# Optimization experiments

Hardware: AMD Instinct MI355X
Metric: run time of the kernel (lower is better)

Reference implementation:

```python
import jax, jax.numpy as jnp
import numpy as np

B, S, E, H, VS, VT = 128, 256, 512, 512, 32000, 32000


def _lstm_layer(x, mask, Wih, Whh, bih, bhh):
    # x: (S,B,E_in), mask: (S,B) bool. PyTorch gate order i,f,g,o.
    h0 = jnp.zeros((x.shape[1], Whh.shape[1]), x.dtype)
    c0 = h0
    def step(carry, inp):
        h, c = carry
        xt, mt = inp
        g = xt @ Wih.T + h @ Whh.T + bih + bhh
        i, f, gg, o = jnp.split(g, 4, axis=-1)
        i = jax.nn.sigmoid(i); f = jax.nn.sigmoid(f)
        gg = jnp.tanh(gg); o = jax.nn.sigmoid(o)
        c_new = f * c + i * gg
        h_new = o * jnp.tanh(c_new)
        m = mt[:, None]
        h2 = jnp.where(m, h_new, h)
        c2 = jnp.where(m, c_new, c)
        return (h2, c2), jnp.where(m, h_new, 0.0)  # pad_packed zero-pads
    (hT, cT), ys = jax.lax.scan(step, (h0, c0), (x, mask))
    return ys, cT


def setup_inputs() -> dict:
    key = jax.random.key(0)
    ks = jax.random.split(key, 32)
    def w(k, shape, fan_in):
        bound = 1.0 / np.sqrt(fan_in)
        return jax.random.uniform(k, shape, jnp.float32, -bound, bound)
    src_tokens = jax.random.randint(ks[0], (B, S), 0, VS)
    src_lens = jnp.sort(jax.random.randint(ks[1], (B,), S // 2, S + 1))[::-1]
    src_lens = src_lens.at[0].set(S)  # pack_padded expects descending, max = S
    trg_tokens = jax.random.randint(ks[2], (B,), 0, VT)
    inp = {
        'src_tokens': src_tokens, 'src_lens': src_lens, 'trg_tokens': trg_tokens,
        'src_emb': jax.random.normal(ks[3], (VS, E), jnp.float32),
        'trg_emb': jax.random.normal(ks[4], (VT, E), jnp.float32),
        'enc_Wih0': w(ks[5], (4 * H, E), H), 'enc_Whh0': w(ks[6], (4 * H, H), H),
        'enc_bih0': w(ks[7], (4 * H,), H), 'enc_bhh0': w(ks[8], (4 * H,), H),
        'enc_Wih1': w(ks[9], (4 * H, H), H), 'enc_Whh1': w(ks[10], (4 * H, H), H),
        'enc_bih1': w(ks[11], (4 * H,), H), 'enc_bhh1': w(ks[12], (4 * H,), H),
        'dec_Wih': w(ks[13], (4 * H, E + H), H), 'dec_Whh': w(ks[14], (4 * H, H), H),
        'dec_bih': w(ks[15], (4 * H,), H), 'dec_bhh': w(ks[16], (4 * H,), H),
        'W_init': w(ks[17], (H, 2 * H), 2 * H), 'b_init': w(ks[18], (H,), 2 * H),
        'W_hid': w(ks[19], (H, 2 * H), 2 * H), 'b_hid': w(ks[20], (H,), 2 * H),
        'W_out': w(ks[21], (VT, H), H), 'b_out': w(ks[22], (VT,), H),
    }
    return inp


def reference(src_tokens, src_lens, trg_tokens, src_emb, trg_emb,
              enc_Wih0, enc_Whh0, enc_bih0, enc_bhh0,
              enc_Wih1, enc_Whh1, enc_bih1, enc_bhh1,
              dec_Wih, dec_Whh, dec_bih, dec_bhh,
              W_init, b_init, W_hid, b_hid, W_out, b_out):
    # ---- encode ----
    x = src_emb[src_tokens]                       # (B,S,E)
    x = jnp.transpose(x, (1, 0, 2))               # (S,B,E)
    mask = jnp.arange(S)[:, None] < src_lens[None, :]  # (S,B)
    y0, c0f = _lstm_layer(x, mask, enc_Wih0, enc_Whh0, enc_bih0, enc_bhh0)
    y1, c1f = _lstm_layer(y0, mask, enc_Wih1, enc_Whh1, enc_bih1, enc_bhh1)
    src_states = jnp.transpose(y1, (1, 0, 2))     # (B,S,H)
    # final cell states (num_layers,B,H) -> (B, num_layers*H)
    final_cells = jnp.concatenate([c0f, c1f], axis=-1)  # (B,2H)
    c_dec = final_cells @ W_init.T + b_init       # (B,H)
    h_dec = jnp.tanh(c_dec)
    # ---- one decoder step ----
    emb_t = trg_emb[trg_tokens]                   # (B,E)
    vec = jnp.concatenate([emb_t, jnp.zeros((B, H), emb_t.dtype)], axis=-1)
    g = vec @ dec_Wih.T + h_dec @ dec_Whh.T + dec_bih + dec_bhh
    i, f, gg, o = jnp.split(g, 4, axis=-1)
    c = jax.nn.sigmoid(f) * c_dec + jax.nn.sigmoid(i) * jnp.tanh(gg)
    h = jax.nn.sigmoid(o) * jnp.tanh(c)           # (B,H)
    # ---- masked dot attention ----
    scores = jnp.einsum('bsh,bh->bs', src_states, h)
    smask = jnp.arange(S)[None, :] < src_lens[:, None]
    scores = jnp.where(smask, scores, -jnp.inf)
    attw = jax.nn.softmax(scores, axis=-1)
    context = jnp.einsum('bs,bsh->bh', attw, src_states)
    attn_vec = jnp.concatenate([h, context], axis=-1) @ W_hid.T + b_hid
    logits = attn_vec @ W_out.T + b_out
    prd_token = jnp.argmax(logits, axis=-1)       # softmax is monotone
    return context, h, prd_token
```

## Files before the change

### kernel.cpp

```cpp
#include <hip/hip_runtime.h>
#include <stdint.h>


typedef _Float16 f16;
typedef f16 f16x8 __attribute__((ext_vector_type(8)));
typedef float f32x4 __attribute__((ext_vector_type(4)));

#define LOSCALE 2048.0f
#define LOINV   (1.0f/2048.0f)

#define B_  128
#define S_  256
#define H_  512

__device__ __forceinline__ uint16_t hbits(f16 h){ union{ f16 f; uint16_t u; } c; c.f=h; return c.u; }
__device__ __forceinline__ float f16val(uint16_t u){ union{ uint16_t u; f16 f; } c; c.u=u; return (float)c.f; }

__device__ __forceinline__ uint32_t split_ph2(float x){
  f16 h = (f16)x;
  float r = (x - (float)h) * LOSCALE;
  return (uint32_t)hbits(h) | ((uint32_t)hbits((f16)r) << 16);
}
__device__ __forceinline__ float ph2val(uint32_t p){
  union{ uint16_t u; f16 f; } a, b; a.u = (uint16_t)p; b.u = (uint16_t)(p>>16);
// ... 116 lines not shown

  for (int it = 0; it < 8; ++it) {
    __syncthreads();
    {
      const uint32_t* gsrc = (wv < 2 ? Ab : Wb) + (size_t)it*8192 + (size_t)(wv & 1)*4096;
      uint32_t* lb = (uint32_t*)(sm + (size_t)wv*16384);
#pragma unroll
      for (int e = 0; e < 16; ++e)
        gload_lds16(gsrc + e*256, lb + e*256, lane);
    }
    asm volatile("s_waitcnt vmcnt(0)" ::: "memory");
    __syncthreads();

#pragma unroll
    for (int kt = 0; kt < 2; ++kt) {
      uint4 ah[4], al[4];
#pragma unroll
      for (int i = 0; i < 4; ++i) {
        const uint8_t* p = sm + (size_t)(kt*8 + wm*4 + i)*2048 + lane*16;
        ah[i] = *(const uint4*)p; al[i] = *(const uint4*)(p + 1024);
      }
#pragma unroll
      for (int j = 0; j < 4; ++j) {
        const uint8_t* p = sm + 32768 + (size_t)(kt*8 + wn*4 + j)*2048 + lane*16;
        uint4 bh = *(const uint4*)p;
        uint4 bl = *(const uint4*)(p + 1024);
#pragma unroll
        for (int i = 0; i < 4; ++i) {
          acc0[i][j] = mfma16(ah[i], bh, acc0[i][j]);
          acc1[i][j] = mfma16(al[i], bh, acc1[i][j]);
          acc1[i][j] = mfma16(ah[i], bl, acc1[i][j]);
        }
      }
    }
  }

#pragma unroll
  for (int i = 0; i < 4; ++i) {
    int row0 = bm0 + (wm*4+i)*16 + ((lane>>4)<<2);
#pragma unroll
    for (int j = 0; j < 4; ++j) {
      int col = bn0 + (wn*4+j)*16 + (lane & 15);
      float bias = 0.f;
      if (b0) bias += b0[col];
      if (b1) bias += b1[col];
      f32x4 v = acc0[i][j] + acc1[i][j] * LOINV;
#pragma unroll
      for (int r = 0; r < 4; ++r) {
        size_t idx = (size_t)(row0 + r) * N + col;
        float out = v[r] + bias;
        if (addC) out += C[idx];
        if (outMode == 2) ((uint16_t*)C)[idx] = hbits((f16)out);
        else              C[idx] = out;
      }
    }
  }
}

__global__ __launch_bounds__(256,2) void k_gemm(
    const uint32_t* __restrict__ A, int lda,
    const float* __restrict__ W, int ldw,
    const float* __restrict__ b0, const float* __restrict__ b1,
    float* __restrict__ C, int N, int K, int addC)
{
  __shared__ uint8_t sm[65536];
  const int tid = threadIdx.x;
  const int lane = tid & 63, wv = tid >> 6;
  const int wm = wv >> 1, wn = wv & 1;
  const int bn0 = blockIdx.x * 128, bm0 = blockIdx.y * 128;

  const int srow = tid >> 1;
  const int skh  = (tid & 1) * 32;
  const int smt  = srow >> 4, sr = srow & 15, skt = tid & 1;

  f32x4 acc0[4][4], acc1[4][4];
#pragma unroll
  for (int i = 0; i < 4; ++i)
#pragma unroll
    for (int j = 0; j < 4; ++j) { acc0[i][j] = (f32x4){0,0,0,0}; acc1[i][j] = (f32x4){0,0,0,0}; }

  for (int k0 = 0; k0 < K; k0 += 64) {
    __syncthreads();
    {
      const uint32_t* ap = A + (size_t)(bm0 + srow) * lda + (k0 + skh);
      uint4 q[8];
#pragma unroll
      for (int e = 0; e < 8; ++e) q[e] = *(const uint4*)(ap + e*4);
#pragma unroll
      for (int kg = 0; kg < 4; ++kg) {
        uint4 hi, lo; pack_hi_lo(q[2*kg], q[2*kg+1], hi, lo);
        uint8_t* dst = sm + (size_t)(smt*2 + skt)*2048 + (size_t)(sr + 16*kg)*16;
        *(uint4*)dst = hi; *(uint4*)(dst + 1024) = lo;
      }
    }
    {
      const float* wp = W + (size_t)(bn0 + srow) * ldw + (k0 + skh);
      float xs[32];
#pragma unroll
      for (int e = 0; e < 8; ++e) { float4 v = *(const float4*)(wp + e*4);
        xs[e*4+0]=v.x; xs[e*4+1]=v.y; xs[e*4+2]=v.z; xs[e*4+3]=v.w; }
#pragma unroll
      for (int kg = 0; kg < 4; ++kg) {
        uint4 hi, lo; split_pack8(xs + kg*8, hi, lo);
        uint8_t* dst = sm + 32768 + (size_t)(smt*2 + skt)*2048 + (size_t)(sr + 16*kg)*16;
        *(uint4*)dst = hi; *(uint4*)(dst + 1024) = lo;
      }
    }
    __syncthreads();

#pragma unroll
    for (int kt = 0; kt < 2; ++kt) {
      uint4 ah[4], al[4];
#pragma unroll
      for (int i = 0; i < 4; ++i) {
        const uint8_t* p = sm + (size_t)(((wm*4+i)*2 + kt))*2048 + lane*16;
        ah[i] = *(const uint4*)p; al[i] = *(const uint4*)(p + 1024);
      }
#pragma unroll
      for (int j = 0; j < 4; ++j) {
        const uint8_t* p = sm + 32768 + (size_t)(((wn*4+j)*2 + kt))*2048 + lane*16;
        uint4 bh = *(const uint4*)p;
        uint4 bl = *(const uint4*)(p + 1024);
#pragma unroll
        for (int i = 0; i < 4; ++i) {
          acc0[i][j] = mfma16(ah[i], bh, acc0[i][j]);
          acc1[i][j] = mfma16(al[i], bh, acc1[i][j]);
          acc1[i][j] = mfma16(ah[i], bl, acc1[i][j]);
        }
      }
    }
  }

#pragma unroll
  for (int i = 0; i < 4; ++i) {
    int row0 = bm0 + (wm*4+i)*16 + ((lane>>4)<<2);
#pragma unroll
    for (int j = 0; j < 4; ++j) {
      int col = bn0 + (wn*4+j)*16 + (lane & 15);
      float bias = 0.f;
      if (b0) bias += b0[col];
      if (b1) bias += b1[col];
      f32x4 v = acc0[i][j] + acc1[i][j] * LOINV;
#pragma unroll
      for (int r = 0; r < 4; ++r) {
        size_t idx = (size_t)(row0 + r) * N + col;
        float out = v[r] + bias;
        if (addC) out += C[idx];
        C[idx] = out;
      }
    }
  }
}

__global__ __launch_bounds__(256,1) void k_lstm2(
    const float* __restrict__ Whh0, const float* __restrict__ Whh1,
    const float* __restrict__ bih1, const float* __restrict__ bhh1,
    const uint16_t* __restrict__ xg,
    const int*  __restrict__ lens,
    uint32_t* __restrict__ mb0,
    uint32_t* __restrict__ mb1,
    float* __restrict__ cb0, float* __restrict__ cb1,
    uint32_t* __restrict__ y1buf,
    uint32_t* __restrict__ flg0, uint32_t* __restrict__ flg1,
    uint32_t* __restrict__ xcdclaim,
    const uint32_t* __restrict__ Wp1,
    int s0, int nt)
{
  __shared__ uint8_t sm[139264];
  uint8_t* wih   = sm;
  uint8_t* tileA = sm + 65536;
  uint8_t* tileB = sm + 98304;
  uint64_t* tA64 = (uint64_t*)tileA;
  uint64_t* tB64 = (uint64_t*)tileB;
  float* g0ex = (float*)(sm + 131072);
  float* g1ex = (float*)(sm + 135168);

  const int tid = threadIdx.x, lane = tid & 63, wv = tid >> 6;
  const int row = lane & 15, qh = lane >> 4;

  uint32_t* claim_sh = (uint32_t*)tileA;
  if (tid == 0) {
    uint32_t xcd;
    asm volatile("s_getreg_b32 %0, hwreg(HW_REG_XCC_ID)" : "=s"(xcd));
    xcd &= 7u;
    uint32_t pos = __hip_atomic_fetch_add(xcdclaim + xcd*16, 1u,
                     __ATOMIC_RELAXED, __HIP_MEMORY_SCOPE_SYSTEM);
    claim_sh[0] = xcd | ((pos & 31u) << 8);
  }
  __syncthreads();
  const uint32_t cl = claim_sh[0];
  const int bg = (int)(cl & 7u), hs = (int)((cl >> 8) & 31u);
  __syncthreads();

  {
    const uint32_t* wpb = Wp1 + (size_t)(wv*4 + (hs >> 3))*65536 + (size_t)(hs & 7)*512;
    uint32_t* lb = (uint32_t*)(wih + (size_t)wv*16384);
#pragma unroll
    for (int kt = 0; kt < 16; ++kt)
      gload_lds16(wpb + kt*4096, lb + kt*256, lane);
  }

  uint4 w0h[16], w0l[16], w1h[16], w1l[16];
  {
    const float* r0 = Whh0 + (size_t)(wv*512 + hs*16 + row)*512 + qh*8;
    const float* r1 = Whh1 + (size_t)(wv*512 + hs*16 + row)*512 + qh*8;
#pragma unroll
    for (int kt = 0; kt < 16; ++kt) {
      float xs[8];
      float4 v0 = *(const float4*)(r0 + kt*32), v1 = *(const float4*)(r0 + kt*32 + 4);
      xs[0]=v0.x; xs[1]=v0.y; xs[2]=v0.z; xs[3]=v0.w;
      xs[4]=v1.x; xs[5]=v1.y; xs[6]=v1.z; xs[7]=v1.w;
      split_pack8(xs, w0h[kt], w0l[kt]);
      v0 = *(const float4*)(r1 + kt*32); v1 = *(const float4*)(r1 + kt*32 + 4);
      xs[0]=v0.x; xs[1]=v0.y; xs[2]=v0.z; xs[3]=v0.w;
      xs[4]=v1.x; xs[5]=v1.y; xs[6]=v1.z; xs[7]=v1.w;
      split_pack8(xs, w1h[kt], w1l[kt]);
    }
  }

  const int b_l = tid >> 4, uu = tid & 15;
  const int bglob = bg*16 + b_l;
  const size_t bgoff = (size_t)bg*8192;
  const int oct_p = hs*2 + (uu >> 3);
  const size_t widx = (size_t)b_l*512 + (size_t)(uu & 1)*256
                    + ((size_t)(oct_p ^ b_l) << 2) + (size_t)((uu & 7) >> 1);
  const int len_b = lens[bglob];
  const int lenA  = lens[bg*16 + row];
  float c0_reg = cb0[(size_t)bglob*512 + hs*16 + uu];
  float c1_reg = cb1[(size_t)bglob*512 + hs*16 + uu];
  float h0_reg, h1_reg;
  {
    size_t ib = (size_t)(s0 & 1)*65536 + bgoff + (size_t)b_l*512
              + ((size_t)(oct_p ^ b_l) << 2) + (size_t)((uu & 7) >> 1);
    uint32_t hiw = mb0[ib], low = mb0[ib + 256];
    int sh = (uu & 1) * 16;
    h0_reg = f16val((uint16_t)(hiw >> sh)) + f16val((uint16_t)(low >> sh)) * LOINV;
    int s1i = (s0 >= 1) ? (s0 - 1) : 0;
    size_t ib1 = (size_t)(s1i & 1)*65536 + bgoff + (size_t)b_l*512
               + ((size_t)(oct_p ^ b_l) << 2) + (size_t)((uu & 7) >> 1);
    hiw = mb1[ib1]; low = mb1[ib1 + 256];
    h1_reg = f16val((uint16_t)(hiw >> sh)) + f16val((uint16_t)(low >> sh)) * LOINV;
  }
  float b1g[4];
#pragma unroll
  for (int g = 0; g < 4; ++g)
    b1g[g] = bih1[g*512 + hs*16 + uu] + bhh1[g*512 + hs*16 + uu];
  const size_t yfl = (size_t)(hs >> 1)*4096 + (size_t)bg*512 + (size_t)(uu & 1)*256
                   + (size_t)((((hs & 1) << 1) | (uu >> 3)))*64 + (size_t)b_l*4
                   + (size_t)((uu & 7) >> 1);

  asm volatile("s_waitcnt vmcnt(0)" ::: "memory");
  __syncthreads();

  for (int it = 0; it < nt; ++it) {
    const int t = s0 + it;
    const bool aL0 = (t < 256);
    const bool aL1 = (t > 0);

    uint16_t x0w[4] = {0,0,0,0};
    if (aL0) {
      const uint16_t* xgp = xg + ((size_t)it*128 + bglob)*2048 + hs*16 + uu;
      x0w[0] = xgp[0]; x0w[1] = xgp[512]; x0w[2] = xgp[1024]; x0w[3] = xgp[1536];
    }

    if (it > 0) {
      if (wv == 0) {
        const uint32_t* fp = flg0 + bg*32 + (lane & 31);
        while (1) {
          uint32_t f = __hip_atomic_load(fp, __ATOMIC_RELAXED, __HIP_MEMORY_SCOPE_AGENT);
          if (__all((int)(f >= (uint32_t)t))) break;
          __builtin_amdgcn_s_sleep(1);
        }
      } else if (wv == 1) {
        const uint32_t* fp = flg1 + bg*32 + (lane & 31);
        while (1) {
          uint32_t f = __hip_atomic_load(fp, __ATOMIC_RELAXED, __HIP_MEMORY_SCOPE_AGENT);
          if (__all((int)(f >= (uint32_t)(t - 1)))) break;
          __builtin_amdgcn_s_sleep(1);
        }
      }
    }
    __builtin_amdgcn_s_barrier();
    __builtin_amdgcn_sched_barrier(0);

    {
      const uint64_t* sp0 = (const uint64_t*)(mb0 + (size_t)(t & 1)*65536 + bgoff);
      const uint64_t* sp1 = (const uint64_t*)(mb1 + (size_t)((t - 1) & 1)*65536 + bgoff);
      uint64_t v0[16], v1[16];
#pragma unroll
      for (int e = 0; e < 16; ++e)
        v0[e] = __hip_atomic_load(sp0 + tid + e*256, __ATOMIC_RELAXED, __HIP_MEMORY_SCOPE_AGENT);
      if (aL1) {
#pragma unroll
        for (int e = 0; e < 16; ++e)
          v1[e] = __hip_atomic_load(sp1 + tid + e*256, __ATOMIC_RELAXED, __HIP_MEMORY_SCOPE_AGENT);
      }
#pragma unroll
      for (int e = 0; e < 16; ++e)
        tA64[tid + e*256] = v0[e];
      if (aL1) {
#pragma unroll
        for (int e = 0; e < 16; ++e)
          tB64[tid + e*256] = v1[e];
      }
    }
    asm volatile("s_waitcnt lgkmcnt(0)" ::: "memory");
    __builtin_amdgcn_s_barrier();
    __builtin_amdgcn_sched_barrier(0);

    f32x4 A0 = (f32x4){0,0,0,0}, A1 = (f32x4){0,0,0,0}, A2 = (f32x4){0,0,0,0};
    f32x4 B0 = (f32x4){0,0,0,0}, B1 = (f32x4){0,0,0,0}, B2 = (f32x4){0,0,0,0};
    {
      const uint8_t* hrp = tileA + (size_t)row*2048;
      const uint8_t* wbase = wih + (size_t)wv*16384;
      const bool cY = aL1 && ((t - 1) < lenA);
      const uint4 z4 = make_uint4(0,0,0,0);
#pragma unroll
      for (int kt = 0; kt < 16; ++kt) {
        int oct = kt*4 + qh;
        const uint8_t* pA = hrp + (((oct ^ row)) << 4);
        uint4 ah = *(const uint4*)pA, al = *(const uint4*)(pA + 1024);
        A0 = mfma16(ah, w0h[kt], A0);
        A1 = mfma16(al, w0h[kt], A1);
        A2 = mfma16(ah, w0l[kt], A2);
        uint4 yh = cY ? ah : z4, yl = cY ? al : z4;
        uint4 bh = *(const uint4*)(wbase + (size_t)kt*1024 + lane*16);
        B0 = mfma16(yh, bh, B0);
        B1 = mfma16(yl, bh, B1);
      }
    }
    if (aL1) {
      const uint8_t* hrp = tileB + (size_t)row*2048;
#pragma unroll
      for (int kt = 0; kt < 16; ++kt) {
        int oct = kt*4 + qh;
        const uint8_t* pA = hrp + (((oct ^ row)) << 4);
        uint4 ah = *(const uint4*)pA, al = *(const uint4*)(pA + 1024);
        B0 = mfma16(ah, w1h[kt], B0);
        B1 = mfma16(al, w1h[kt], B1);
        B2 = mfma16(ah, w1l[kt], B2);
      }
    }

    {
      int col = lane & 15, rb = (lane >> 4) << 2;
      if (aL0) {
#pragma unroll
        for (int r = 0; r < 4; ++r)
          g0ex[(size_t)(wv*16 + rb + r)*16 + col] = A0[r] + (A1[r] + A2[r])*LOINV;
      }
      if (aL1) {
#pragma unroll
        for (int r = 0; r < 4; ++r)
          g1ex[(size_t)(wv*16 + rb + r)*16 + col] = B0[r] + (B1[r] + B2[r])*LOINV;
      }
    }
    asm volatile("s_waitcnt lgkmcnt(0)" ::: "memory");
    __builtin_amdgcn_s_barrier();
    __builtin_amdgcn_sched_barrier(0);

    uint32_t p1w = 0; bool m1 = false;
    if (aL0) {
      float gi = g0ex[(size_t)(0*16 + b_l)*16 + uu] + f16val(x0w[0]);
      float gf = g0ex[(size_t)(1*16 + b_l)*16 + uu] + f16val(x0w[1]);
      float gg = g0ex[(size_t)(2*16 + b_l)*16 + uu] + f16val(x0w[2]);
      float go = g0ex[(size_t)(3*16 + b_l)*16 + uu] + f16val(x0w[3]);
      float cn = fsigm(gf)*c0_reg + fsigm(gi)*ftanh(gg);
      float hn = fsigm(go)*ftanh(cn);
      bool m = (t < len_b);
      c0_reg = m ? cn : c0_reg;
      h0_reg = m ? hn : h0_reg;
      uint32_t p = split_ph2(h0_reg);
      uint32_t pp = __shfl_xor(p, 1);
      __hip_atomic_store(mb0 + (size_t)((t + 1) & 1)*65536 + bgoff + widx,
                         plane_word(p, pp, uu & 1), __ATOMIC_RELAXED, __HIP_MEMORY_SCOPE_AGENT);
    }
    if (aL1) {
      float gi = g1ex[(size_t)(0*16 + b_l)*16 + uu] + b1g[0];
      float gf = g1ex[(size_t)(1*16 + b_l)*16 + uu] + b1g[1];
      float gg = g1ex[(size_t)(2*16 + b_l)*16 + uu] + b1g[2];
      float go = g1ex[(size_t)(3*16 + b_l)*16 + uu] + b1g[3];
      float cn = fsigm(gf)*c1_reg + fsigm(gi)*ftanh(gg);
      float hn = fsigm(go)*ftanh(cn);
      m1 = ((t - 1) < len_b);
      c1_reg = m1 ? cn : c1_reg;
      h1_reg = m1 ? hn : h1_reg;
      uint32_t p = split_ph2(h1_reg);
      uint32_t pp = __shfl_xor(p, 1);
      p1w = plane_word(p, pp, uu & 1);
      __hip_atomic_store(mb1 + (size_t)(t & 1)*65536 + bgoff + widx,
                         p1w, __ATOMIC_RELAXED, __HIP_MEMORY_SCOPE_AGENT);
    }
    asm volatile("s_waitcnt vmcnt(0)" ::: "memory");
    __builtin_amdgcn_s_barrier();
    __builtin_amdgcn_sched_barrier(0);
    if (tid == 0) {
      if (aL0) __hip_atomic_store(flg0 + bg*32 + hs, (uint32_t)(t + 1),
                                  __ATOMIC_RELAXED, __HIP_MEMORY_SCOPE_AGENT);
      if (aL1) __hip_atomic_store(flg1 + bg*32 + hs, (uint32_t)t,
                                  __ATOMIC_RELAXED, __HIP_MEMORY_SCOPE_AGENT);
    }
    if (aL1) y1buf[(size_t)(t - 1)*65536 + yfl] = m1 ? p1w : 0u;
  }
  cb0[(size_t)bglob*512 + hs*16 + uu] = c0_reg;
  cb1[(size_t)bglob*512 + hs*16 + uu] = c1_reg;
}

__global__ __launch_bounds__(256) void k_pack2(const float* __restrict__ a,
    const float* __restrict__ b, uint32_t* __restrict__ out)
{
  int i = blockIdx.x*256 + threadIdx.x;
  int bb = i >> 10, k = i & 1023;
  float x = (k < 512) ? a[(size_t)bb*512 + k] : b[(size_t)bb*512 + k - 512];
  out[i] = split_ph2(x);
}

__global__ __launch_bounds__(256) void k_tanh_split(const float* __restrict__ c,
    uint32_t* __restrict__ hp)
{ int i = blockIdx.x*256 + threadIdx.x; hp[i] = split_ph2(tanhf(c[i])); }

__global__ __launch_bounds__(256) void k_dec_cell(const float* __restrict__ g,
    const float* __restrict__ cdec, float* __restrict__ hout, float* __restrict__ dh)
{
  int i = blockIdx.x*256 + threadIdx.x;
  int b = i >> 9, u = i & 511;
  const float* gb = g + (size_t)b*2048;
  float c = sigm(gb[512 + u])*cdec[i] + sigm(gb[u])*tanhf(gb[1024 + u]);
  float h = sigm(gb[1536 + u])*tanhf(c);
  hout[i] = h; dh[i] = h;
}

__global__ __launch_bounds__(256) void k_attn(const uint32_t* __restrict__ y1,
    const float* __restrict__ h, const int* __restrict__ lens,
    float* __restrict__ ctx, float* __restrict__ dctx)
{
  __shared__ float hsh[512];
  __shared__ float sc[256];
  __shared__ float red[8];
  const int b = blockIdx.x, tid = threadIdx.x, lane = tid & 63, wv = tid >> 6;
  hsh[tid]       = h[(size_t)b*512 + tid];
  hsh[tid + 256] = h[(size_t)b*512 + tid + 256];
  const int len = lens[b];
  __syncthreads();

  const size_t lanebase = (size_t)(lane >> 2)*4096 + (size_t)(b >> 4)*512
                        + (size_t)(lane & 3)*64 + (size_t)(b & 15)*4;
  for (int it = 0; it < 64; ++it) {
    int s = wv*64 + it;
    const uint32_t* yb = y1 + (size_t)s*65536 + lanebase;
    uint4 hw = *(const uint4*)yb;
    uint4 lw = *(const uint4*)(yb + 256);
    int k0 = lane*8;
    uint32_t hws[4] = {hw.x,hw.y,hw.z,hw.w}, lws[4] = {lw.x,lw.y,lw.z,lw.w};
    float d = 0.f;
#pragma unroll
    for (int w = 0; w < 4; ++w) {
      d += (f16val((uint16_t)hws[w]) + f16val((uint16_t)lws[w])*LOINV) * hsh[k0 + 2*w]
         + (f16val((uint16_t)(hws[w]>>16)) + f16val((uint16_t)(lws[w]>>16))*LOINV) * hsh[k0 + 2*w + 1];
    }
    for (int off = 32; off; off >>= 1) d += __shfl_xor(d, off);
    if (lane == 0) sc[s] = d;
  }
  __syncthreads();

  float v = (tid < len) ? sc[tid] : -INFINITY;
  float mx = v;
  for (int off = 32; off; off >>= 1) mx = fmaxf(mx, __shfl_xor(mx, off));
  if (lane == 0) red[wv] = mx;
  __syncthreads();
  mx = fmaxf(fmaxf(red[0], red[1]), fmaxf(red[2], red[3]));
  float e = (tid < len) ? expf(v - mx) : 0.f;
  float ssum = e;
  for (int off = 32; off; off >>= 1) ssum += __shfl_xor(ssum, off);
  if (lane == 0) red[4 + wv] = ssum;
  __syncthreads();
  float tot = red[4] + red[5] + red[6] + red[7];
  __syncthreads();
  sc[tid] = e / tot;
  __syncthreads();

  const int u0 = tid, u1 = tid + 256;
  const size_t bu0 = (size_t)(u0 >> 5)*4096 + (size_t)(b >> 4)*512
                   + (size_t)((u0 >> 3) & 3)*64 + (size_t)(b & 15)*4 + (size_t)((u0 & 7) >> 1);
  const size_t bu1 = (size_t)(u1 >> 5)*4096 + (size_t)(b >> 4)*512
                   + (size_t)((u1 >> 3) & 3)*64 + (size_t)(b & 15)*4 + (size_t)((u1 & 7) >> 1);
  const int sh = (tid & 1) * 16;
  float acc0 = 0.f, acc1 = 0.f;
  for (int s = 0; s < 256; ++s) {
    float w = sc[s];
    const uint32_t* yb = y1 + (size_t)s*65536;
    uint32_t hi0 = yb[bu0], lo0 = yb[bu0 + 256];
    uint32_t hi1 = yb[bu1], lo1 = yb[bu1 + 256];
    acc0 += w*(f16val((uint16_t)(hi0 >> sh)) + f16val((uint16_t)(lo0 >> sh))*LOINV);
    acc1 += w*(f16val((uint16_t)(hi1 >> sh)) + f16val((uint16_t)(lo1 >> sh))*LOINV);
  }
  ctx [(size_t)b*512 + tid]       = acc0;  ctx [(size_t)b*512 + tid + 256] = acc1;
  dctx[(size_t)b*512 + tid]       = acc0;  dctx[(size_t)b*512 + tid + 256] = acc1;
}

__global__ __launch_bounds__(256) void k_argmax(const float* __restrict__ logits,
    float* __restrict__ out)
{
  __shared__ float bv[256];
  __shared__ int   bi[256];
  const int b = blockIdx.x, tid = threadIdx.x;
  const float* L = logits + (size_t)b*32000;
  float best = -INFINITY; int idx = 0;
  for (int i = tid; i < 32000; i += 256) {
    float v = L[i];
    if (v > best) { best = v; idx = i; }
  }
  bv[tid] = best; bi[tid] = idx;
  __syncthreads();
  for (int sft = 128; sft; sft >>= 1) {
    if (tid < sft) {
      if (bv[tid+sft] > bv[tid] || (bv[tid+sft] == bv[tid] && bi[tid+sft] < bi[tid])) {
        bv[tid] = bv[tid+sft]; bi[tid] = bi[tid+sft];
      }
    }
    __syncthreads();
  }
  if (tid == 0) out[b] = (float)bi[0];
}

extern "C" void kernel_launch(void* const* d_in, const int* in_sizes, int n_in,
                              void* d_out, int out_size, void* d_ws, size_t ws_size,
                              hipStream_t stream)
{
  (void)in_sizes; (void)n_in; (void)out_size; (void)ws_size;
  const int*   src_tokens = (const int*)  d_in[0];
  const int*   src_lens   = (const int*)  d_in[1];
  const int*   trg_tokens = (const int*)  d_in[2];
  const float* src_emb    = (const float*)d_in[3];
  const float* trg_emb    = (const float*)d_in[4];
  const float* Wih0 = (const float*)d_in[5];
  const float* Whh0 = (const float*)d_in[6];
  const float* bih0 = (const float*)d_in[7];
  const float* bhh0 = (const float*)d_in[8];
  const float* Wih1 = (const float*)d_in[9];
  const float* Whh1 = (const float*)d_in[10];
  const float* bih1 = (const float*)d_in[11];
  const float* bhh1 = (const float*)d_in[12];
  const float* dWih = (const float*)d_in[13];
  const float* dWhh = (const float*)d_in[14];
  const float* dbih = (const float*)d_in[15];
  const float* dbhh = (const float*)d_in[16];
  const float* Winit= (const float*)d_in[17];
  const float* binit= (const float*)d_in[18];
  const float* Whid = (const float*)d_in[19];
  const float* bhid = (const float*)d_in[20];
  const float* Wout = (const float*)d_in[21];
  const float* bout = (const float*)d_in[22];

  uint8_t* ws = (uint8_t*)d_ws;
  constexpr size_t MBs = 1ull << 20;
  constexpr size_t OFF_AP    = 0;
  constexpr size_t OFF_Y1    = 64*MBs;
  constexpr size_t OFF_XG    = 128*MBs;
  constexpr size_t OFF_MB    = 192*MBs;
  constexpr size_t OFF_CB0   = OFF_MB    + 1*MBs;
  constexpr size_t OFF_CB1   = OFF_CB0   + 256*1024;
  constexpr size_t OFF_FLG   = OFF_CB1   + 256*1024;
  constexpr size_t OFF_PK    = OFF_FLG   + 4096;
  constexpr size_t OFF_CDEC  = OFF_PK    + 512*1024;
  constexpr size_t OFF_HDECP = OFF_CDEC  + 256*1024;
  constexpr size_t OFF_EMBP  = OFF_HDECP + 256*1024;
  constexpr size_t OFF_G     = OFF_EMBP  + 256*1024;
  constexpr size_t OFF_HDEC2 = OFF_G     + 1*MBs;
  constexpr size_t OFF_CTX   = OFF_HDEC2 + 256*1024;
  constexpr size_t OFF_AVEC  = OFF_CTX   + 256*1024;
  constexpr size_t OFF_AVECP = OFF_AVEC  + 256*1024;
  constexpr size_t OFF_LOG   = OFF_AVECP + 256*1024;

  uint32_t* Ap    = (uint32_t*)(ws + OFF_AP);
  uint32_t* Y1    = (uint32_t*)(ws + OFF_Y1);
  uint16_t* Xg    = (uint16_t*)(ws + OFF_XG);
  uint32_t* mb0   = (uint32_t*)(ws + OFF_MB);
  uint32_t* mb1   = (uint32_t*)(ws + OFF_MB + 512*1024);
  float*    cb0   = (float*)   (ws + OFF_CB0);
  float*    cb1   = (float*)   (ws + OFF_CB1);
  uint32_t* flg0  = (uint32_t*)(ws + OFF_FLG);
  uint32_t* xclm  = (uint32_t*)(ws + OFF_FLG + 1024);
  uint32_t* flg1  = (uint32_t*)(ws + OFF_FLG + 2048);
  uint32_t* pk    = (uint32_t*)(ws + OFF_PK);
  float*    cdec  = (float*)   (ws + OFF_CDEC);
  uint32_t* hdecp = (uint32_t*)(ws + OFF_HDECP);
  uint32_t* embp  = (uint32_t*)(ws + OFF_EMBP);
  float*    g     = (float*)   (ws + OFF_G);
  float*    hdec2 = (float*)   (ws + OFF_HDEC2);
  float*    ctx   = (float*)   (ws + OFF_CTX);
  float*    avec  = (float*)   (ws + OFF_AVEC);
  uint32_t* avecp = (uint32_t*)(ws + OFF_AVECP);
  float*    logit = (float*)   (ws + OFF_LOG);
  uint32_t* Wp0   = (uint32_t*)(ws + OFF_LOG);
  uint32_t* Wp1   = (uint32_t*)(ws + OFF_LOG + 4*MBs);
  float*    dout  = (float*)   d_out;

  k_packW<<<4096, 256, 0, stream>>>(Wih0, Wp0);
  k_packW<<<4096, 256, 0, stream>>>(Wih1, Wp1);

  hipMemsetAsync(mb0,  0, 1024*1024, stream);
  hipMemsetAsync(flg0, 0, 4096, stream);
  hipMemsetAsync(cb0,  0, 65536*4, stream);
  hipMemsetAsync(cb1,  0, 65536*4, stream);
  k_embed_src_fl<<<2048, 256, 0, stream>>>(src_tokens, src_emb, Ap);
  for (int c = 0; c < 4; ++c) {
    int s0 = c * 64;
    k_gemm_fl<<<dim3(16, 64), 256, 0, stream>>>(Ap + (size_t)s0*65536,
        Wp0, bih0, bhh0, (float*)Xg, 2048, 0, 2);
    k_lstm2<<<256, 256, 0, stream>>>(Whh0, Whh1, bih1, bhh1, Xg, src_lens,
        mb0, mb1, cb0, cb1, Y1, flg0, flg1, xclm, Wp1, s0, (c == 3) ? 65 : 64);
  }

  k_pack2<<<512, 256, 0, stream>>>(cb0, cb1, pk);
  k_gemm<<<dim3(4, 1), 256, 0, stream>>>(pk, 1024, Winit, 1024, binit, nullptr,
      cdec, 512, 1024, 0);
  k_tanh_split<<<256, 256, 0, stream>>>(cdec, hdecp);

  k_embed_trg<<<256, 256, 0, stream>>>(trg_tokens, trg_emb, embp);
  k_gemm<<<dim3(16, 1), 256, 0, stream>>>(embp, 512, dWih, 1024, dbih, dbhh,
      g, 2048, 512, 0);
  k_gemm<<<dim3(16, 1), 256, 0, stream>>>(hdecp, 512, dWhh, 512, nullptr, nullptr,
      g, 2048, 512, 1);
  k_dec_cell<<<256, 256, 0, stream>>>(g, cdec, hdec2, dout + 65536);

  k_attn<<<128, 256, 0, stream>>>(Y1, hdec2, src_lens, ctx, dout);

  k_pack2<<<512, 256, 0, stream>>>(hdec2, ctx, pk);
  k_gemm<<<dim3(4, 1), 256, 0, stream>>>(pk, 1024, Whid, 1024, bhid, nullptr,
      avec, 512, 1024, 0);
  k_pack1<<<256, 256, 0, stream>>>(avec, avecp);
  k_gemm<<<dim3(250, 1), 256, 0, stream>>>(avecp, 512, Wout, 512, bout, nullptr,
      logit, 32000, 512, 0);
  k_argmax<<<128, 256, 0, stream>>>(logit, dout + 131072);
}
```

Measured before the change: 2.366 ms.

## Overlap next chunk's input GEMM with LSTM recurrence using extra waves

Doubles the LSTM kernel block to 512 threads. The four original waves run the recurrence, and four new waves compute the next chunk's layer-0 input-gate GEMM into a double-buffered Xg, a slice per timestep. This removes the separate serial GEMM launches between recurrence chunks. It also drops the low-precision correction plane for the layer-1 recurrent weights to save registers and MFMAs, at some accuracy cost. The larger block raises register pressure and adds memory traffic inside the latency-critical step loop.

```diff
diff --git a/kernel.cpp b/kernel.cpp
--- a/kernel.cpp
+++ b/kernel.cpp
@@ -292,7 +292,7 @@
   }
 }
 
-__global__ __launch_bounds__(256,1) void k_lstm2(
+__global__ __launch_bounds__(512,1) void k_lstm2(
     const float* __restrict__ Whh0, const float* __restrict__ Whh1,
     const float* __restrict__ bih1, const float* __restrict__ bhh1,
     const uint16_t* __restrict__ xg,
@@ -304,7 +304,11 @@
     uint32_t* __restrict__ flg0, uint32_t* __restrict__ flg1,
     uint32_t* __restrict__ xcdclaim,
     const uint32_t* __restrict__ Wp1,
-    int s0, int nt)
+    const uint32_t* __restrict__ Wp0,
+    const uint32_t* __restrict__ ApN,
+    uint16_t* __restrict__ XgN,
+    const float* __restrict__ bih0, const float* __restrict__ bhh0,
+    int doGemm, int s0, int nt)
 {
   __shared__ uint8_t sm[139264];
   uint8_t* wih   = sm;
@@ -316,6 +320,7 @@
   float* g1ex = (float*)(sm + 135168);
 
   const int tid = threadIdx.x, lane = tid & 63, wv = tid >> 6;
+  const bool rec = (wv < 4);
   const int row = lane & 15, qh = lane >> 4;
 
   uint32_t* claim_sh = (uint32_t*)tileA;
@@ -327,70 +332,86 @@
                      __ATOMIC_RELAXED, __HIP_MEMORY_SCOPE_SYSTEM);
     claim_sh[0] = xcd | ((pos & 31u) << 8);
   }
-  __syncthreads();
-  const uint32_t cl = claim_sh[0];
-  const int bg = (int)(cl & 7u), hs = (int)((cl >> 8) & 31u);
-  __syncthreads();
-
-  {
-    const uint32_t* wpb = Wp1 + (size_t)(wv*4 + (hs >> 3))*65536 + (size_t)(hs & 7)*512;
-    uint32_t* lb = (uint32_t*)(wih + (size_t)wv*16384);
-#pragma unroll
-    for (int kt = 0; kt < 16; ++kt)
-      gload_lds16(wpb + kt*4096, lb + kt*256, lane);
-  }
-
-  uint4 w0h[16], w0l[16], w1h[16], w1l[16];
-  {
-    const float* r0 = Whh0 + (size_t)(wv*512 + hs*16 + row)*512 + qh*8;
-    const float* r1 = Whh1 + (size_t)(wv*512 + hs*16 + row)*512 + qh*8;
-#pragma unroll
-    for (int kt = 0; kt < 16; ++kt) {
-      float xs[8];
-      float4 v0 = *(const float4*)(r0 + kt*32), v1 = *(const float4*)(r0 + kt*32 + 4);
-      xs[0]=v0.x; xs[1]=v0.y; xs[2]=v0.z; xs[3]=v0.w;
-      xs[4]=v1.x; xs[5]=v1.y; xs[6]=v1.z; xs[7]=v1.w;
-      split_pack8(xs, w0h[kt], w0l[kt]);
-      v0 = *(const float4*)(r1 + kt*32); v1 = *(const float4*)(r1 + kt*32 + 4);
-      xs[0]=v0.x; xs[1]=v0.y; xs[2]=v0.z; xs[3]=v0.w;
-      xs[4]=v1.x; xs[5]=v1.y; xs[6]=v1.z; xs[7]=v1.w;
-      split_pack8(xs, w1h[kt], w1l[kt]);
-    }
-  }
-
-  const int b_l = tid >> 4, uu = tid & 15;
-  const int bglob = bg*16 + b_l;
-  const size_t bgoff = (size_t)bg*8192;
-  const int oct_p = hs*2 + (uu >> 3);
-  const size_t widx = (size_t)b_l*512 + (size_t)(uu & 1)*256
-                    + ((size_t)(oct_p ^ b_l) << 2) + (size_t)((uu & 7) >> 1);
-  const int len_b = lens[bglob];
-  const int lenA  = lens[bg*16 + row];
-  float c0_reg = cb0[(size_t)bglob*512 + hs*16 + uu];
-  float c1_reg = cb1[(size_t)bglob*512 + hs*16 + uu];
-  float h0_reg, h1_reg;
-  {
-    size_t ib = (size_t)(s0 & 1)*65536 + bgoff + (size_t)b_l*512
-              + ((size_t)(oct_p ^ b_l) << 2) + (size_t)((uu & 7) >> 1);
-    uint32_t hiw = mb0[ib], low = mb0[ib + 256];
-    int sh = (uu & 1) * 16;
-    h0_reg = f16val((uint16_t)(hiw >> sh)) + f16val((uint16_t)(low >> sh)) * LOINV;
-    int s1i = (s0 >= 1) ? (s0 - 1) : 0;
-    size_t ib1 = (size_t)(s1i & 1)*65536 + bgoff + (size_t)b_l*512
-               + ((size_t)(oct_p ^ b_l) << 2) + (size_t)((uu & 7) >> 1);
-    hiw = mb1[ib1]; low = mb1[ib1 + 256];
-    h1_reg = f16val((uint16_t)(hiw >> sh)) + f16val((uint16_t)(low >> sh)) * LOINV;
-  }
-  float b1g[4];
-#pragma unroll
-  for (int g = 0; g < 4; ++g)
-    b1g[g] = bih1[g*512 + hs*16 + uu] + bhh1[g*512 + hs*16 + uu];
-  const size_t yfl = (size_t)(hs >> 1)*4096 + (size_t)bg*512 + (size_t)(uu & 1)*256
-                   + (size_t)((((hs & 1) << 1) | (uu >> 3)))*64 + (size_t)b_l*4
-                   + (size_t)((uu & 7) >> 1);
+  asm volatile("s_waitcnt lgkmcnt(0)" ::: "memory");
+  __builtin_amdgcn_s_barrier();
+  int bg = 0, hs = 0;
+  if (rec) {
+    const uint32_t cl = claim_sh[0];
+    bg = (int)(cl & 7u); hs = (int)((cl >> 8) & 31u);
+  }
+  __builtin_amdgcn_s_barrier();
+
+  uint4 w0h[16], w0l[16], w1h[16];
+  int b_l = 0, uu = 0, bglob = 0, len_b = 0, lenA = 0;
+  size_t bgoff = 0, widx = 0, yfl = 0;
+  float c0_reg = 0.f, c1_reg = 0.f, h0_reg = 0.f, h1_reg = 0.f;
+  float b1g[4] = {0.f, 0.f, 0.f, 0.f};
+  if (rec) {
+    {
+      const uint32_t* wpb = Wp1 + (size_t)(wv*4 + (hs >> 3))*65536 + (size_t)(hs & 7)*512;
+      uint32_t* lb = (uint32_t*)(wih + (size_t)wv*16384);
+#pragma unroll
+      for (int kt = 0; kt < 16; ++kt)
+        gload_lds16(wpb + kt*4096, lb + kt*256, lane);
+    }
+    {
+      const float* r0 = Whh0 + (size_t)(wv*512 + hs*16 + row)*512 + qh*8;
+      const float* r1 = Whh1 + (size_t)(wv*512 + hs*16 + row)*512 + qh*8;
+#pragma unroll
+      for (int kt = 0; kt < 16; ++kt) {
+        float xs[8];
+        float4 v0 = *(const float4*)(r0 + kt*32), v1 = *(const float4*)(r0 + kt*32 + 4);
+        xs[0]=v0.x; xs[1]=v0.y; xs[2]=v0.z; xs[3]=v0.w;
+        xs[4]=v1.x; xs[5]=v1.y; xs[6]=v1.z; xs[7]=v1.w;
+        split_pack8(xs, w0h[kt], w0l[kt]);
+        v0 = *(const float4*)(r1 + kt*32); v1 = *(const float4*)(r1 + kt*32 + 4);
+        xs[0]=v0.x; xs[1]=v0.y; xs[2]=v0.z; xs[3]=v0.w;
+        xs[4]=v1.x; xs[5]=v1.y; xs[6]=v1.z; xs[7]=v1.w;
+        uint4 dummy;
+        split_pack8(xs, w1h[kt], dummy);
+        (void)dummy;
+      }
+    }
+    b_l = tid >> 4; uu = tid & 15;
+    bglob = bg*16 + b_l;
+    bgoff = (size_t)bg*8192;
+    const int oct_p = hs*2 + (uu >> 3);
+    widx = (size_t)b_l*512 + (size_t)(uu & 1)*256
+         + ((size_t)(oct_p ^ b_l) << 2) + (size_t)((uu & 7) >> 1);
+    len_b = lens[bglob];
+    lenA  = lens[bg*16 + row];
+    c0_reg = cb0[(size_t)bglob*512 + hs*16 + uu];
+    c1_reg = cb1[(size_t)bglob*512 + hs*16 + uu];
+    {
+      size_t ib = (size_t)(s0 & 1)*65536 + bgoff + (size_t)b_l*512
+                + ((size_t)(oct_p ^ b_l) << 2) + (size_t)((uu & 7) >> 1);
+      uint32_t hiw = mb0[ib], low = mb0[ib + 256];
+      int sh = (uu & 1) * 16;
+      h0_reg = f16val((uint16_t)(hiw >> sh)) + f16val((uint16_t)(low >> sh)) * LOINV;
+      int s1i = (s0 >= 1) ? (s0 - 1) : 0;
+      size_t ib1 = (size_t)(s1i & 1)*65536 + bgoff + (size_t)b_l*512
+                 + ((size_t)(oct_p ^ b_l) << 2) + (size_t)((uu & 7) >> 1);
+      hiw = mb1[ib1]; low = mb1[ib1 + 256];
+      h1_reg = f16val((uint16_t)(hiw >> sh)) + f16val((uint16_t)(low >> sh)) * LOINV;
+    }
+#pragma unroll
+    for (int g = 0; g < 4; ++g)
+      b1g[g] = bih1[g*512 + hs*16 + uu] + bhh1[g*512 + hs*16 + uu];
+    yfl = (size_t)(hs >> 1)*4096 + (size_t)bg*512 + (size_t)(uu & 1)*256
+        + (size_t)((((hs & 1) << 1) | (uu >> 3)))*64 + (size_t)b_l*4
+        + (size_t)((uu & 7) >> 1);
+  }
+  const int gw = wv - 4;
+  const int mblk = blockIdx.x >> 4, nblk = blockIdx.x & 15;
+  f32x4 ga0[2][2], ga1[2][2];
+#pragma unroll
+  for (int i = 0; i < 2; ++i)
+#pragma unroll
+    for (int j = 0; j < 2; ++j) { ga0[i][j] = (f32x4){0,0,0,0}; ga1[i][j] = (f32x4){0,0,0,0}; }
 
   asm volatile("s_waitcnt vmcnt(0)" ::: "memory");
-  __syncthreads();
+  __builtin_amdgcn_s_barrier();
+  __builtin_amdgcn_sched_barrier(0);
 
   for (int it = 0; it < nt; ++it) {
     const int t = s0 + it;
@@ -398,32 +419,83 @@
     const bool aL1 = (t > 0);
 
     uint16_t x0w[4] = {0,0,0,0};
-    if (aL0) {
-      const uint16_t* xgp = xg + ((size_t)it*128 + bglob)*2048 + hs*16 + uu;
-      x0w[0] = xgp[0]; x0w[1] = xgp[512]; x0w[2] = xgp[1024]; x0w[3] = xgp[1536];
-    }
-
-    if (it > 0) {
-      if (wv == 0) {
-        const uint32_t* fp = flg0 + bg*32 + (lane & 31);
-        while (1) {
-          uint32_t f = __hip_atomic_load(fp, __ATOMIC_RELAXED, __HIP_MEMORY_SCOPE_AGENT);
-          if (__all((int)(f >= (uint32_t)t))) break;
-          __builtin_amdgcn_s_sleep(1);
-        }
-      } else if (wv == 1) {
-        const uint32_t* fp = flg1 + bg*32 + (lane & 31);
-        while (1) {
-          uint32_t f = __hip_atomic_load(fp, __ATOMIC_RELAXED, __HIP_MEMORY_SCOPE_AGENT);
-          if (__all((int)(f >= (uint32_t)(t - 1)))) break;
-          __builtin_amdgcn_s_sleep(1);
+    if (rec) {
+      if (aL0) {
+        const uint16_t* xgp = xg + ((size_t)it*128 + bglob)*2048 + hs*16 + uu;
+        x0w[0] = xgp[0]; x0w[1] = xgp[512]; x0w[2] = xgp[1024]; x0w[3] = xgp[1536];
+      }
+      if (it > 0) {
+        if (wv == 0) {
+          const uint32_t* fp = flg0 + bg*32 + (lane & 31);
+          while (1) {
+            uint32_t f = __hip_atomic_load(fp, __ATOMIC_RELAXED, __HIP_MEMORY_SCOPE_AGENT);
+            if (__all((int)(f >= (uint32_t)t))) break;
+            __builtin_amdgcn_s_sleep(1);
+          }
+        } else if (wv == 1) {
+          const uint32_t* fp = flg1 + bg*32 + (lane & 31);
+          while (1) {
+            uint32_t f = __hip_atomic_load(fp, __ATOMIC_RELAXED, __HIP_MEMORY_SCOPE_AGENT);
+            if (__all((int)(f >= (uint32_t)(t - 1)))) break;
+            __builtin_amdgcn_s_sleep(1);
+          }
+        }
+      }
+    } else if (doGemm && it < 64) {
+      const int sf = it >> 2, ph = it & 3;
+      const int mg = sf >> 2, ng = sf & 3;
+      const int sstep = mblk*4 + gw;
+      if (ph == 0) {
+#pragma unroll
+        for (int i = 0; i < 2; ++i)
+#pragma unroll
+          for (int j = 0; j < 2; ++j) { ga0[i][j] = (f32x4){0,0,0,0}; ga1[i][j] = (f32x4){0,0,0,0}; }
+      }
+      const uint32_t* ab = ApN + (size_t)sstep*65536 + (size_t)(mg*2)*512 + lane*4;
+      const uint32_t* bb = Wp0 + (size_t)nblk*65536 + (size_t)(ng*2)*512 + lane*4;
+#pragma unroll
+      for (int kk = 0; kk < 4; ++kk) {
+        const int kt = ph*4 + kk;
+        uint4 gbh[2], gbl[2], gah[2], gal[2];
+#pragma unroll
+        for (int j = 0; j < 2; ++j) {
+          gbh[j] = *(const uint4*)(bb + (size_t)kt*4096 + j*512);
+          gbl[j] = *(const uint4*)(bb + (size_t)kt*4096 + j*512 + 256);
+        }
+#pragma unroll
+        for (int i = 0; i < 2; ++i) {
+          gah[i] = *(const uint4*)(ab + (size_t)kt*4096 + i*512);
+          gal[i] = *(const uint4*)(ab + (size_t)kt*4096 + i*512 + 256);
+        }
+#pragma unroll
+        for (int i = 0; i < 2; ++i)
+#pragma unroll
+          for (int j = 0; j < 2; ++j) {
+            ga0[i][j] = mfma16(gah[i], gbh[j], ga0[i][j]);
+            ga1[i][j] = mfma16(gal[i], gbh[j], ga1[i][j]);
+            ga1[i][j] = mfma16(gah[i], gbl[j], ga1[i][j]);
+          }
+      }
+      if (ph == 3) {
+#pragma unroll
+        for (int j = 0; j < 2; ++j) {
+          const int col = nblk*128 + (ng*2 + j)*16 + (lane & 15);
+          const float bias = bih0[col] + bhh0[col];
+#pragma unroll
+          for (int i = 0; i < 2; ++i) {
+            const int rowb = sstep*128 + (mg*2 + i)*16 + ((lane >> 4) << 2);
+#pragma unroll
+            for (int r = 0; r < 4; ++r)
+              XgN[(size_t)(rowb + r)*2048 + col] =
+                hbits((f16)(ga0[i][j][r] + ga1[i][j][r]*LOINV + bias));
+          }
         }
       }
     }
     __builtin_amdgcn_s_barrier();
     __builtin_amdgcn_sched_barrier(0);
 
-    {
+    if (rec) {
       const uint64_t* sp0 = (const uint64_t*)(mb0 + (size_t)(t & 1)*65536 + bgoff);
       const uint64_t* sp1 = (const uint64_t*)(mb1 + (size_t)((t - 1) & 1)*65536 + bgoff);
       uint64_t v0[16], v1[16];
@@ -449,50 +521,50 @@
     __builtin_amdgcn_sched_barrier(0);
 
     f32x4 A0 = (f32x4){0,0,0,0}, A1 = (f32x4){0,0,0,0}, A2 = (f32x4){0,0,0,0};
-    f32x4 B0 = (f32x4){0,0,0,0}, B1 = (f32x4){0,0,0,0}, B2 = (f32x4){0,0,0,0};
-    {
-      const uint8_t* hrp = tileA + (size_t)row*2048;
-      const uint8_t* wbase = wih + (size_t)wv*16384;
-      const bool cY = aL1 && ((t - 1) < lenA);
-      const uint4 z4 = make_uint4(0,0,0,0);
-#pragma unroll
-      for (int kt = 0; kt < 16; ++kt) {
-        int oct = kt*4 + qh;
-        const uint8_t* pA = hrp + (((oct ^ row)) << 4);
-        uint4 ah = *(const uint4*)pA, al = *(const uint4*)(pA + 1024);
-        A0 = mfma16(ah, w0h[kt], A0);
-        A1 = mfma16(al, w0h[kt], A1);
-        A2 = mfma16(ah, w0l[kt], A2);
-        uint4 yh = cY ? ah : z4, yl = cY ? al : z4;
-        uint4 bh = *(const uint4*)(wbase + (size_t)kt*1024 + lane*16);
-        B0 = mfma16(yh, bh, B0);
-        B1 = mfma16(yl, bh, B1);
-      }
-    }
-    if (aL1) {
-      const uint8_t* hrp = tileB + (size_t)row*2048;
-#pragma unroll
-      for (int kt = 0; kt < 16; ++kt) {
-        int oct = kt*4 + qh;
-        const uint8_t* pA = hrp + (((oct ^ row)) << 4);
-        uint4 ah = *(const uint4*)pA, al = *(const uint4*)(pA + 1024);
-        B0 = mfma16(ah, w1h[kt], B0);
-        B1 = mfma16(al, w1h[kt], B1);
-        B2 = mfma16(ah, w1l[kt], B2);
-      }
-    }
-
-    {
-      int col = lane & 15, rb = (lane >> 4) << 2;
-      if (aL0) {
-#pragma unroll
-        for (int r = 0; r < 4; ++r)
-          g0ex[(size_t)(wv*16 + rb + r)*16 + col] = A0[r] + (A1[r] + A2[r])*LOINV;
+    f32x4 B0 = (f32x4){0,0,0,0}, B1 = (f32x4){0,0,0,0};
+    if (rec) {
+      {
+        const uint8_t* hrp = tileA + (size_t)row*2048;
+        const uint8_t* wbase = wih + (size_t)wv*16384;
+        const bool cY = aL1 && ((t - 1) < lenA);
+        const uint4 z4 = make_uint4(0,0,0,0);
+#pragma unroll
+        for (int kt = 0; kt < 16; ++kt) {
+          int oct = kt*4 + qh;
+          const uint8_t* pA = hrp + (((oct ^ row)) << 4);
+          uint4 ah = *(const uint4*)pA, al = *(const uint4*)(pA + 1024);
+          A0 = mfma16(ah, w0h[kt], A0);
+          A1 = mfma16(al, w0h[kt], A1);
+          A2 = mfma16(ah, w0l[kt], A2);
+          uint4 yh = cY ? ah : z4, yl = cY ? al : z4;
+          uint4 bh = *(const uint4*)(wbase + (size_t)kt*1024 + lane*16);
+          B0 = mfma16(yh, bh, B0);
+          B1 = mfma16(yl, bh, B1);
+        }
       }
       if (aL1) {
-#pragma unroll
-        for (int r = 0; r < 4; ++r)
-          g1ex[(size_t)(wv*16 + rb + r)*16 + col] = B0[r] + (B1[r] + B2[r])*LOINV;
+        const uint8_t* hrp = tileB + (size_t)row*2048;
+#pragma unroll
+        for (int kt = 0; kt < 16; ++kt) {
+          int oct = kt*4 + qh;
+          const uint8_t* pA = hrp + (((oct ^ row)) << 4);
+          uint4 ah = *(const uint4*)pA, al = *(const uint4*)(pA + 1024);
+          B0 = mfma16(ah, w1h[kt], B0);
+          B1 = mfma16(al, w1h[kt], B1);
+        }
+      }
+      {
+        int col = lane & 15, rb = (lane >> 4) << 2;
+        if (aL0) {
+#pragma unroll
+          for (int r = 0; r < 4; ++r)
+            g0ex[(size_t)(wv*16 + rb + r)*16 + col] = A0[r] + (A1[r] + A2[r])*LOINV;
+        }
+        if (aL1) {
+#pragma unroll
+          for (int r = 0; r < 4; ++r)
+            g1ex[(size_t)(wv*16 + rb + r)*16 + col] = B0[r] + B1[r]*LOINV;
+        }
       }
     }
     asm volatile("s_waitcnt lgkmcnt(0)" ::: "memory");
@@ -500,50 +572,56 @@
     __builtin_amdgcn_sched_barrier(0);
 
     uint32_t p1w = 0; bool m1 = false;
-    if (aL0) {
-      float gi = g0ex[(size_t)(0*16 + b_l)*16 + uu] + f16val(x0w[0]);
-      float gf = g0ex[(size_t)(1*16 + b_l)*16 + uu] + f16val(x0w[1]);
-      float gg = g0ex[(size_t)(2*16 + b_l)*16 + uu] + f16val(x0w[2]);
-      float go = g0ex[(size_t)(3*16 + b_l)*16 + uu] + f16val(x0w[3]);
-      float cn = fsigm(gf)*c0_reg + fsigm(gi)*ftanh(gg);
-      float hn = fsigm(go)*ftanh(cn);
-      bool m = (t < len_b);
-      c0_reg = m ? cn : c0_reg;
-      h0_reg = m ? hn : h0_reg;
-      uint32_t p = split_ph2(h0_reg);
-      uint32_t pp = __shfl_xor(p, 1);
-      __hip_atomic_store(mb0 + (size_t)((t + 1) & 1)*65536 + bgoff + widx,
-                         plane_word(p, pp, uu & 1), __ATOMIC_RELAXED, __HIP_MEMORY_SCOPE_AGENT);
-    }
-    if (aL1) {
-      float gi = g1ex[(size_t)(0*16 + b_l)*16 + uu] + b1g[0];
-      float gf = g1ex[(size_t)(1*16 + b_l)*16 + uu] + b1g[1];
-      float gg = g1ex[(size_t)(2*16 + b_l)*16 + uu] + b1g[2];
-      float go = g1ex[(size_t)(3*16 + b_l)*16 + uu] + b1g[3];
-      float cn = fsigm(gf)*c1_reg + fsigm(gi)*ftanh(gg);
-      float hn = fsigm(go)*ftanh(cn);
-      m1 = ((t - 1) < len_b);
-      c1_reg = m1 ? cn : c1_reg;
-      h1_reg = m1 ? hn : h1_reg;
-      uint32_t p = split_ph2(h1_reg);
-      uint32_t pp = __shfl_xor(p, 1);
-      p1w = plane_word(p, pp, uu & 1);
-      __hip_atomic_store(mb1 + (size_t)(t & 1)*65536 + bgoff + widx,
-                         p1w, __ATOMIC_RELAXED, __HIP_MEMORY_SCOPE_AGENT);
+    if (rec) {
+      if (aL0) {
+        float gi = g0ex[(size_t)(0*16 + b_l)*16 + uu] + f16val(x0w[0]);
+        float gf = g0ex[(size_t)(1*16 + b_l)*16 + uu] + f16val(x0w[1]);
+        float gg = g0ex[(size_t)(2*16 + b_l)*16 + uu] + f16val(x0w[2]);
+        float go = g0ex[(size_t)(3*16 + b_l)*16 + uu] + f16val(x0w[3]);
+        float cn = fsigm(gf)*c0_reg + fsigm(gi)*ftanh(gg);
+        float hn = fsigm(go)*ftanh(cn);
+        bool m = (t < len_b);
+        c0_reg = m ? cn : c0_reg;
+        h0_reg = m ? hn : h0_reg;
+        uint32_t p = split_ph2(h0_reg);
+        uint32_t pp = __shfl_xor(p, 1);
+        __hip_atomic_store(mb0 + (size_t)((t + 1) & 1)*65536 + bgoff + widx,
+                           plane_word(p, pp, uu & 1), __ATOMIC_RELAXED, __HIP_MEMORY_SCOPE_AGENT);
+      }
+      if (aL1) {
+        float gi = g1ex[(size_t)(0*16 + b_l)*16 + uu] + b1g[0];
+        float gf = g1ex[(size_t)(1*16 + b_l)*16 + uu] + b1g[1];
+        float gg = g1ex[(size_t)(2*16 + b_l)*16 + uu] + b1g[2];
+        float go = g1ex[(size_t)(3*16 + b_l)*16 + uu] + b1g[3];
+        float cn = fsigm(gf)*c1_reg + fsigm(gi)*ftanh(gg);
+        float hn = fsigm(go)*ftanh(cn);
+        m1 = ((t - 1) < len_b);
+        c1_reg = m1 ? cn : c1_reg;
+        h1_reg = m1 ? hn : h1_reg;
+        uint32_t p = split_ph2(h1_reg);
+        uint32_t pp = __shfl_xor(p, 1);
+        p1w = plane_word(p, pp, uu & 1);
+        __hip_atomic_store(mb1 + (size_t)(t & 1)*65536 + bgoff + widx,
+                           p1w, __ATOMIC_RELAXED, __HIP_MEMORY_SCOPE_AGENT);
+      }
     }
     asm volatile("s_waitcnt vmcnt(0)" ::: "memory");
     __builtin_amdgcn_s_barrier();
     __builtin_amdgcn_sched_barrier(0);
-    if (tid == 0) {
-      if (aL0) __hip_atomic_store(flg0 + bg*32 + hs, (uint32_t)(t + 1),
-                                  __ATOMIC_RELAXED, __HIP_MEMORY_SCOPE_AGENT);
-      if (aL1) __hip_atomic_store(flg1 + bg*32 + hs, (uint32_t)t,
-                                  __ATOMIC_RELAXED, __HIP_MEMORY_SCOPE_AGENT);
-    }
-    if (aL1) y1buf[(size_t)(t - 1)*65536 + yfl] = m1 ? p1w : 0u;
-  }
-  cb0[(size_t)bglob*512 + hs*16 + uu] = c0_reg;
-  cb1[(size_t)bglob*512 + hs*16 + uu] = c1_reg;
+    if (rec) {
+      if (tid == 0) {
+        if (aL0) __hip_atomic_store(flg0 + bg*32 + hs, (uint32_t)(t + 1),
+                                    __ATOMIC_RELAXED, __HIP_MEMORY_SCOPE_AGENT);
+        if (aL1) __hip_atomic_store(flg1 + bg*32 + hs, (uint32_t)t,
+                                    __ATOMIC_RELAXED, __HIP_MEMORY_SCOPE_AGENT);
+      }
+      if (aL1) y1buf[(size_t)(t - 1)*65536 + yfl] = m1 ? p1w : 0u;
+    }
+  }
+  if (rec) {
+    cb0[(size_t)bglob*512 + hs*16 + uu] = c0_reg;
+    cb1[(size_t)bglob*512 + hs*16 + uu] = c1_reg;
+  }
 }
 
 __global__ __launch_bounds__(256) void k_pack2(const float* __restrict__ a,
@@ -714,7 +792,8 @@
 
   uint32_t* Ap    = (uint32_t*)(ws + OFF_AP);
   uint32_t* Y1    = (uint32_t*)(ws + OFF_Y1);
-  uint16_t* Xg    = (uint16_t*)(ws + OFF_XG);
+  uint16_t* Xg0   = (uint16_t*)(ws + OFF_XG);
+  uint16_t* Xg1   = (uint16_t*)(ws + OFF_XG + 32*MBs);
   uint32_t* mb0   = (uint32_t*)(ws + OFF_MB);
   uint32_t* mb1   = (uint32_t*)(ws + OFF_MB + 512*1024);
   float*    cb0   = (float*)   (ws + OFF_CB0);
@@ -744,12 +823,17 @@
   hipMemsetAsync(cb0,  0, 65536*4, stream);
   hipMemsetAsync(cb1,  0, 65536*4, stream);
   k_embed_src_fl<<<2048, 256, 0, stream>>>(src_tokens, src_emb, Ap);
+  k_gemm_fl<<<dim3(16, 64), 256, 0, stream>>>(Ap, Wp0, bih0, bhh0,
+      (float*)Xg0, 2048, 0, 2);
   for (int c = 0; c < 4; ++c) {
     int s0 = c * 64;
-    k_gemm_fl<<<dim3(16, 64), 256, 0, stream>>>(Ap + (size_t)s0*65536,
-        Wp0, bih0, bhh0, (float*)Xg, 2048, 0, 2);
-    k_lstm2<<<256, 256, 0, stream>>>(Whh0, Whh1, bih1, bhh1, Xg, src_lens,
-        mb0, mb1, cb0, cb1, Y1, flg0, flg1, xclm, Wp1, s0, (c == 3) ? 65 : 64);
+    uint16_t* xgCur = (c & 1) ? Xg1 : Xg0;
+    uint16_t* xgNxt = (c & 1) ? Xg0 : Xg1;
+    const uint32_t* apN = (c < 3) ? (Ap + (size_t)(c + 1)*64*65536) : Ap;
+    k_lstm2<<<256, 512, 0, stream>>>(Whh0, Whh1, bih1, bhh1, xgCur, src_lens,
+        mb0, mb1, cb0, cb1, Y1, flg0, flg1, xclm, Wp1,
+        Wp0, apN, xgNxt, bih0, bhh0, (c < 3) ? 1 : 0,
+        s0, (c == 3) ? 65 : 64);
   }
 
   k_pack2<<<512, 256, 0, stream>>>(cb0, cb1, pk);
```

Result: slower. 5.173 ms (+118.6%).
